# Kernel optimization log

Hardware: AMD Instinct MI355X
Metric: run time of the kernel (lower is better)

Reference implementation:

```python
import jax, jax.numpy as jnp
import numpy as np
import math

EMBED = 256
HEADS = 4
HEAD_DIM = EMBED // HEADS
OUT_DIM = 256
LN_EPS = 1e-5


def _qkv_init(key):
    # diagonal-domination init from Galerkin Transformer (Cao): U(-spread,spread)*gain + delta*I
    spread = math.sqrt(3.0 / EMBED)
    gain, delta = 0.01, 0.01
    w = jax.random.uniform(key, (EMBED, EMBED), minval=-spread, maxval=spread) * gain
    return w + delta * jnp.eye(EMBED, dtype=w.dtype)


def setup_inputs() -> dict:
    key = jax.random.key(0)
    ks = jax.random.split(key, 6)
    seq = jax.random.normal(ks[0], (4, 8192, EMBED), dtype=jnp.float32)
    wq = _qkv_init(ks[1])
    wk = _qkv_init(ks[2])
    wv = _qkv_init(ks[3])
    # nn.Linear default init for wo
    bound = 1.0 / math.sqrt(EMBED)
    wo = jax.random.uniform(ks[4], (OUT_DIM, EMBED), minval=-bound, maxval=bound)
    bo = jax.random.uniform(ks[5], (OUT_DIM,), minval=-bound, maxval=bound)
    ln_k_g = jnp.ones((HEAD_DIM,), jnp.float32)
    ln_k_b = jnp.zeros((HEAD_DIM,), jnp.float32)
    ln_v_g = jnp.ones((HEAD_DIM,), jnp.float32)
    ln_v_b = jnp.zeros((HEAD_DIM,), jnp.float32)
    return {"seq": seq, "wq": wq, "wk": wk, "wv": wv, "wo": wo, "bo": bo,
            "ln_k_g": ln_k_g, "ln_k_b": ln_k_b, "ln_v_g": ln_v_g, "ln_v_b": ln_v_b}


def _layer_norm(x, g, b):
    mu = jnp.mean(x, axis=-1, keepdims=True)
    var = jnp.mean(jnp.square(x - mu), axis=-1, keepdims=True)
    return (x - mu) * jax.lax.rsqrt(var + LN_EPS) * g + b


def _split_heads(x, B, S):
    # [B, S, E] -> [B, H, S, D]
    return x.reshape(B, S, HEADS, HEAD_DIM).transpose(0, 2, 1, 3)


def reference(seq, wq, wk, wv, wo, bo, ln_k_g, ln_k_b, ln_v_g, ln_v_b):
    B, S, _ = seq.shape
    q = _split_heads(seq @ wq.T, B, S)
    k = _split_heads(seq @ wk.T, B, S)
    v = _split_heads(seq @ wv.T, B, S)
    k = _layer_norm(k, ln_k_g, ln_k_b)
    v = _layer_norm(v, ln_v_g, ln_v_b)
    # Galerkin (softmax-free) attention: Q @ (K^T V) / n  -- O(n d^2)
    kv = jnp.einsum('bhsd,bhse->bhde', k, v) / S   # [B,H,D,D]
    ga = jnp.einsum('bhsd,bhde->bhse', q, kv)       # [B,H,S,D]
    ga = ga.transpose(0, 2, 1, 3).reshape(B, S, EMBED)
    return ga @ wo.T + bo
```

## Files before the change

### kernel.cpp

```cpp
#include <hip/hip_runtime.h>
#include <stdint.h>


#define EMBED 256
#define SEQ   8192
#define LN_EPS 1e-5f

using bf16x8 = __attribute__((ext_vector_type(8))) short;
using bf16x4 = __attribute__((ext_vector_type(4))) short;
using f32x4  = __attribute__((ext_vector_type(4))) float;

static __device__ __forceinline__ short f2bf(float f) {
  uint32_t x = __float_as_uint(f);
  uint32_t r = x + 0x7fffu + ((x >> 16) & 1u);
  return (short)(r >> 16);
}
static __device__ __forceinline__ float bf2f(uint32_t u) {
  return __uint_as_float(u << 16);
}

#define MFMA16(a, b, c) __builtin_amdgcn_mfma_f32_16x16x32_bf16((a), (b), (c), 0, 0, 0)

template <int ROWS>
static __device__ __forceinline__ void stage_x(char* smem, const float* __restrict__ src, int tid) {
#pragma unroll
  for (int i = 0; i < ROWS / 8; ++i) {
    int g = tid + i * 256;
    int row = g >> 5, c16 = g & 31;
    const f32x4* p = (const f32x4*)(src + row * EMBED + c16 * 8);
    f32x4 f0 = p[0], f1 = p[1];
    bf16x8 v;
    v[0] = f2bf(f0[0]); v[1] = f2bf(f0[1]); v[2] = f2bf(f0[2]); v[3] = f2bf(f0[3]);
    v[4] = f2bf(f1[0]); v[5] = f2bf(f1[1]); v[6] = f2bf(f1[2]); v[7] = f2bf(f1[3]);
    *(bf16x8*)(smem + row * 512 + ((c16 * 16) ^ ((row & 7) << 4))) = v;
  }
}

__global__ void gka_prep(const float* __restrict__ wq, const float* __restrict__ wk,
                         const float* __restrict__ wv, const float* __restrict__ wo,
                         unsigned short* __restrict__ wkf, unsigned short* __restrict__ wvf,
                         unsigned short* __restrict__ wqt, unsigned short* __restrict__ wob) {
  int blk = blockIdx.x, tid = threadIdx.x;
  if (blk < 64) {
    int g = (blk & 31) * 256 + tid;
    const float* W = (blk < 32) ? wk : wv;
    unsigned short* D = (blk < 32) ? wkf : wvf;
    int wid = g >> 11, kk = (g >> 8) & 7, n = (g >> 6) & 3, ln = g & 63;
    int row = wid * 64 + n * 16 + (ln & 15);
    int c0 = kk * 32 + (ln >> 4) * 8;
    const f32x4* p = (const f32x4*)(W + row * 256 + c0);
    f32x4 f0 = p[0], f1 = p[1];
    bf16x8 v;
    v[0] = f2bf(f0[0]); v[1] = f2bf(f0[1]); v[2] = f2bf(f0[2]); v[3] = f2bf(f0[3]);
    v[4] = f2bf(f1[0]); v[5] = f2bf(f1[1]); v[6] = f2bf(f1[2]); v[7] = f2bf(f1[3]);
    *(bf16x8*)(D + g * 8) = v;
  } else if (blk < 320) {
    int e = (blk - 64) * 256 + tid;
    int i = e >> 8, j = e & 255;
    wqt[e] = (unsigned short)f2bf(wq[j * 256 + i]);
  } else {
    int e = (blk - 320) * 256 + tid;
    wob[e] = (unsigned short)f2bf(wo[e]);
  }
}

__global__ __launch_bounds__(256, 2)
void gka_kv(const float* __restrict__ seq,
            const unsigned short* __restrict__ wkf, const unsigned short* __restrict__ wvf,
            const float* __restrict__ lkg, const float* __restrict__ lkb,
            const float* __restrict__ lvg, const float* __restrict__ lvb,
            unsigned short* __restrict__ P) {
  __shared__ char smem[65536];
  const int tid = threadIdx.x;
  const int lane = tid & 63;
  const int wid = tid >> 6;
  const int l15 = lane & 15, l4 = lane >> 4, l7 = lane & 7;
  const int tile = blockIdx.x;
  const int b = tile >> 7;
  const int ptile = tile & 127;

  stage_x<64>(smem, seq + (size_t)(b * SEQ + ptile * 64) * EMBED, tid);
  __syncthreads();

#pragma unroll
  for (int mat = 0; mat < 2; ++mat) {
    const unsigned short* Wf = mat ? wvf : wkf;
    const float* gp = mat ? lvg : lkg;
    const float* bp = mat ? lvb : lkb;
    float gv[4], bv[4];
#pragma unroll
    for (int n = 0; n < 4; ++n) { gv[n] = gp[n * 16 + l15]; bv[n] = bp[n * 16 + l15]; }

    f32x4 acc[4][4];
#pragma unroll
    for (int m = 0; m < 4; ++m)
#pragma unroll
      for (int n = 0; n < 4; ++n) acc[m][n] = (f32x4)0.0f;

#pragma unroll
    for (int kk = 0; kk < 8; ++kk) {
      bf16x8 af[4], bw[4];
#pragma unroll
      for (int m = 0; m < 4; ++m) {
        int row = m * 16 + l15;
        af[m] = *(const bf16x8*)(smem + row * 512 + ((kk * 64 + l4 * 16) ^ (l7 << 4)));
      }
#pragma unroll
      for (int n = 0; n < 4; ++n)
        bw[n] = *(const bf16x8*)(Wf + ((((wid * 8 + kk) * 4 + n) * 64 + lane) << 3));
#pragma unroll
      for (int m = 0; m < 4; ++m)
#pragma unroll
        for (int n = 0; n < 4; ++n)
          acc[m][n] = MFMA16(af[m], bw[n], acc[m][n]);
    }

    if (mat == 1) __syncthreads();

    char* T = smem + (mat ? 0 : 32768) + wid * 8192;
#pragma unroll
    for (int m = 0; m < 4; ++m) {
      float mu[4], rs[4];
#pragma unroll
      for (int r = 0; r < 4; ++r) {
        float s1 = 0.f, s2 = 0.f;
#pragma unroll
        for (int n = 0; n < 4; ++n) { float x = acc[m][n][r]; s1 += x; s2 += x * x; }
#pragma unroll
        for (int msk = 1; msk < 16; msk <<= 1) {
          s1 += __shfl_xor(s1, msk);
          s2 += __shfl_xor(s2, msk);
        }
        mu[r] = s1 * (1.f / 64.f);
        float var = s2 * (1.f / 64.f) - mu[r] * mu[r];
        rs[r] = rsqrtf(var + LN_EPS);
      }
#pragma unroll
      for (int n = 0; n < 4; ++n) {
        bf16x4 pk;
#pragma unroll
        for (int r = 0; r < 4; ++r)
          pk[r] = f2bf((acc[m][n][r] - mu[r]) * rs[r] * gv[n] + bv[n]);
        int d = n * 16 + l15;
        int sb = m * 32 + l4 * 8;
        *(bf16x4*)(T + d * 128 + (sb ^ (l7 << 4))) = pk;
      }
    }
  }

  __syncthreads();

  f32x4 a2[4][4];
#pragma unroll
  for (int fd = 0; fd < 4; ++fd)
#pragma unroll
    for (int n = 0; n < 4; ++n) a2[fd][n] = (f32x4)0.0f;

#pragma unroll
  for (int kk = 0; kk < 2; ++kk) {
    bf16x8 ak[4], bv2[4];
#pragma unroll
    for (int fd = 0; fd < 4; ++fd) {
      int d = fd * 16 + l15;
      ak[fd] = *(const bf16x8*)(smem + 32768 + wid * 8192 + d * 128 +
                                ((kk * 64 + l4 * 16) ^ (l7 << 4)));
    }
#pragma unroll
    for (int n = 0; n < 4; ++n) {
      int e = n * 16 + l15;
      bv2[n] = *(const bf16x8*)(smem + wid * 8192 + e * 128 +
                                ((kk * 64 + l4 * 16) ^ (l7 << 4)));
    }
#pragma unroll
    for (int fd = 0; fd < 4; ++fd)
#pragma unroll
      for (int n = 0; n < 4; ++n)
        a2[fd][n] = MFMA16(ak[fd], bv2[n], a2[fd][n]);
  }

  unsigned short* Ph = P + ((size_t)((b * 128 + ptile) * 4 + wid) << 12);
#pragma unroll
  for (int fd = 0; fd < 4; ++fd)
#pragma unroll
    for (int n = 0; n < 4; ++n) {
      bf16x4 pk;
#pragma unroll
      for (int r = 0; r < 4; ++r) pk[r] = f2bf(a2[fd][n][r]);
      *(bf16x4*)(Ph + (fd * 4 + n) * 256 + lane * 4) = pk;
    }
}

__global__ __launch_bounds__(128)
void gka_red(const unsigned short* __restrict__ P, float* __restrict__ kvf) {
  int q = blockIdx.x * 128 + threadIdx.x;
  int b = q >> 12, h = (q >> 10) & 3, t4 = q & 1023;
  const unsigned short* p0 = P + ((size_t)(b * 128) * 4 + h) * 4096 + t4 * 4;
  float s0 = 0.f, s1 = 0.f, s2 = 0.f, s3 = 0.f;
#pragma unroll 4
  for (int p = 0; p < 128; ++p) {
    uint2 u = *(const uint2*)(p0 + (size_t)p * 16384);
    s0 += bf2f(u.x & 0xffffu); s1 += bf2f(u.x >> 16);
    s2 += bf2f(u.y & 0xffffu); s3 += bf2f(u.y >> 16);
  }
  f32x4 r; r[0] = s0; r[1] = s1; r[2] = s2; r[3] = s3;
  *(f32x4*)(kvf + ((b * 4 + h) << 12) + t4 * 4) = r;
}

__global__ __launch_bounds__(256, 2)
void gka_m1(const float* __restrict__ kvf, const unsigned short* __restrict__ wob,
            unsigned short* __restrict__ m1t) {
  const int tid = threadIdx.x;
  const int lane = tid & 63;
  const int wid = tid >> 6;
  const int l15 = lane & 15, l4 = lane >> 4;
  const int blk = blockIdx.x;
  const int b = blk >> 2, h = blk & 3;
  const float invS = 1.f / (float)SEQ;
  const float* kvh = kvf + ((b * 4 + h) << 12);

  f32x4 acc[4][4];
#pragma unroll
  for (int m = 0; m < 4; ++m)
#pragma unroll
    for (int n = 0; n < 4; ++n) acc[m][n] = (f32x4)0.0f;

#pragma unroll
  for (int kk = 0; kk < 2; ++kk) {
    bf16x8 af[4], bw[4];
#pragma unroll
    for (int m = 0; m < 4; ++m) {
      int base = (m * 4 + kk * 2 + (l4 >> 1)) * 256 +
                 ((l15 >> 2) * 16 + (l4 & 1) * 8) * 4 + (l15 & 3);
      bf16x8 v;
#pragma unroll
      for (int j = 0; j < 8; ++j) v[j] = f2bf(kvh[base + j * 4] * invS);
      af[m] = v;
    }
#pragma unroll
    for (int n = 0; n < 4; ++n) {
      int o = wid * 64 + n * 16 + l15;
      bw[n] = *(const bf16x8*)(wob + o * 256 + h * 64 + kk * 32 + l4 * 8);
    }
#pragma unroll
    for (int m = 0; m < 4; ++m)
#pragma unroll
      for (int n = 0; n < 4; ++n)
        acc[m][n] = MFMA16(af[m], bw[n], acc[m][n]);
  }
#pragma unroll
  for (int m = 0; m < 4; ++m)
#pragma unroll
    for (int n = 0; n < 4; ++n) {
      int o = wid * 64 + n * 16 + l15;
      int j0 = h * 64 + m * 16 + l4 * 4;
      bf16x4 pk;
#pragma unroll
      for (int r = 0; r < 4; ++r) pk[r] = f2bf(acc[m][n][r]);
      *(bf16x4*)(m1t + (size_t)(b * 256 + o) * 256 + j0) = pk;
    }
}

__global__ __launch_bounds__(512, 2)
void gka_wc(const unsigned short* __restrict__ wqt, const unsigned short* __restrict__ m1t,
            unsigned short* __restrict__ wcf) {
  const int tid = threadIdx.x;
  const int lane = tid & 63;
  const int wid = tid >> 6;
  const int wm = wid >> 2, wn = wid & 3;
  const int l15 = lane & 15, l4 = lane >> 4;
  const int blk = blockIdx.x;
  const int b = blk >> 1, ih = blk & 1;

  f32x4 acc[4][4];
#pragma unroll
  for (int m = 0; m < 4; ++m)
#pragma unroll
    for (int n = 0; n < 4; ++n) acc[m][n] = (f32x4)0.0f;

#pragma unroll
  for (int kk = 0; kk < 8; ++kk) {
    bf16x8 af[4], bw[4];
#pragma unroll
    for (int m = 0; m < 4; ++m) {
      int i = ih * 128 + wm * 64 + m * 16 + l15;
      af[m] = *(const bf16x8*)(wqt + i * 256 + kk * 32 + l4 * 8);
    }
#pragma unroll
    for (int n = 0; n < 4; ++n) {
      int o = wn * 64 + n * 16 + l15;
      bw[n] = *(const bf16x8*)(m1t + (size_t)(b * 256 + o) * 256 + kk * 32 + l4 * 8);
    }
#pragma unroll
    for (int m = 0; m < 4; ++m)
#pragma unroll
      for (int n = 0; n < 4; ++n)
        acc[m][n] = MFMA16(af[m], bw[n], acc[m][n]);
  }
#pragma unroll
  for (int m = 0; m < 4; ++m)
#pragma unroll
    for (int n = 0; n < 4; ++n) {
      int kko = ih * 4 + wm * 2 + (m >> 1);
      int laneo = ((m & 1) * 2 + (l4 >> 1)) * 16 + l15;
      int jo = (l4 & 1) * 4;
      bf16x4 pk;
#pragma unroll
      for (int r = 0; r < 4; ++r) pk[r] = f2bf(acc[m][n][r]);
      *(bf16x4*)(wcf + ((size_t)b << 16) +
                 (((((wn * 8 + kko) * 4 + n) * 64) + laneo) << 3) + jo) = pk;
    }
}

__global__ __launch_bounds__(256, 4)
void gka_out(const float* __restrict__ seq, const unsigned short* __restrict__ wcf,
             const float* __restrict__ bo, float* __restrict__ out) {
  __shared__ char smem[16384];
  const int tid = threadIdx.x;
  const int lane = tid & 63;
  const int wid = tid >> 6;
  const int l15 = lane & 15, l4 = lane >> 4, l7 = lane & 7;
  const int tile = blockIdx.x;
  const int b = tile >> 8;
  const int srow = (tile & 255) * 32;

  stage_x<32>(smem, seq + (size_t)(b * SEQ + srow) * EMBED, tid);

  const unsigned short* Wf = wcf + ((size_t)b << 16);
  float bov[4];
#pragma unroll
  for (int n = 0; n < 4; ++n) bov[n] = bo[wid * 64 + n * 16 + l15];

  f32x4 acc[2][4];
#pragma unroll
  for (int m = 0; m < 2; ++m)
#pragma unroll
    for (int n = 0; n < 4; ++n) acc[m][n] = (f32x4)0.0f;

  __syncthreads();

#pragma unroll
  for (int kk = 0; kk < 8; ++kk) {
    bf16x8 af[2], bw[4];
#pragma unroll
    for (int m = 0; m < 2; ++m) {
      int row = m * 16 + l15;
      af[m] = *(const bf16x8*)(smem + row * 512 + ((kk * 64 + l4 * 16) ^ (l7 << 4)));
    }
#pragma unroll
    for (int n = 0; n < 4; ++n)
      bw[n] = *(const bf16x8*)(Wf + ((((wid * 8 + kk) * 4 + n) * 64 + lane) << 3));
#pragma unroll
    for (int m = 0; m < 2; ++m)
#pragma unroll
      for (int n = 0; n < 4; ++n)
        acc[m][n] = MFMA16(af[m], bw[n], acc[m][n]);
  }

  float* dst = out + (size_t)(b * SEQ + srow) * EMBED;
#pragma unroll
  for (int m = 0; m < 2; ++m)
#pragma unroll
    for (int n = 0; n < 4; ++n)
#pragma unroll
      for (int r = 0; r < 4; ++r)
        dst[(size_t)(m * 16 + l4 * 4 + r) * EMBED + wid * 64 + n * 16 + l15] =
            acc[m][n][r] + bov[n];
}

extern "C" void kernel_launch(void* const* d_in, const int* in_sizes, int n_in,
                              void* d_out, int out_size, void* d_ws, size_t ws_size,
                              hipStream_t stream) {
  const float* seq = (const float*)d_in[0];
  const float* wq  = (const float*)d_in[1];
  const float* wk  = (const float*)d_in[2];
  const float* wv  = (const float*)d_in[3];
  const float* wo  = (const float*)d_in[4];
  const float* bo  = (const float*)d_in[5];
  const float* lkg = (const float*)d_in[6];
  const float* lkb = (const float*)d_in[7];
  const float* lvg = (const float*)d_in[8];
  const float* lvb = (const float*)d_in[9];
  float* out = (float*)d_out;
  char* ws = (char*)d_ws;

  unsigned short* wkf = (unsigned short*)(ws + 0);
  unsigned short* wvf = (unsigned short*)(ws + 131072);
  unsigned short* wqt = (unsigned short*)(ws + 262144);
  unsigned short* wob = (unsigned short*)(ws + 393216);
  float*          kvf = (float*)(ws + 524288);
  unsigned short* m1t = (unsigned short*)(ws + 786432);
  unsigned short* wcf = (unsigned short*)(ws + 1310720);
  unsigned short* P   = (unsigned short*)d_out;

  gka_prep<<<576, 256, 0, stream>>>(wq, wk, wv, wo, wkf, wvf, wqt, wob);
  gka_kv<<<512, 256, 0, stream>>>(seq, wkf, wvf, lkg, lkb, lvg, lvb, P);
  gka_red<<<128, 128, 0, stream>>>(P, kvf);
  gka_m1<<<16, 256, 0, stream>>>(kvf, wob, m1t);
  gka_wc<<<8, 512, 0, stream>>>(wqt, m1t, wcf);
  gka_out<<<1024, 256, 0, stream>>>(seq, wcf, bo, out);
}
```

Baseline: 79.78 us.

## Tile wq transpose, split partial reduction, fuse wo conversion, drop LDS staging in output

```diff
diff --git a/kernel.cpp b/kernel.cpp
--- a/kernel.cpp
+++ b/kernel.cpp
@@ -1,4 +1,5 @@
 #include <hip/hip_runtime.h>
+#include <hip/hip_bf16.h>
 #include <stdint.h>
 
 
@@ -11,9 +12,8 @@
 using f32x4  = __attribute__((ext_vector_type(4))) float;
 
 static __device__ __forceinline__ short f2bf(float f) {
-  uint32_t x = __float_as_uint(f);
-  uint32_t r = x + 0x7fffu + ((x >> 16) & 1u);
-  return (short)(r >> 16);
+  __hip_bfloat16 h = __float2bfloat16(f);
+  return __builtin_bit_cast(short, h);
 }
 static __device__ __forceinline__ float bf2f(uint32_t u) {
   return __uint_as_float(u << 16);
@@ -21,10 +21,9 @@
 
 #define MFMA16(a, b, c) __builtin_amdgcn_mfma_f32_16x16x32_bf16((a), (b), (c), 0, 0, 0)
 
-template <int ROWS>
 static __device__ __forceinline__ void stage_x(char* smem, const float* __restrict__ src, int tid) {
 #pragma unroll
-  for (int i = 0; i < ROWS / 8; ++i) {
+  for (int i = 0; i < 8; ++i) {
     int g = tid + i * 256;
     int row = g >> 5, c16 = g & 31;
     const f32x4* p = (const f32x4*)(src + row * EMBED + c16 * 8);
@@ -37,9 +36,10 @@
 }
 
 __global__ void gka_prep(const float* __restrict__ wq, const float* __restrict__ wk,
-                         const float* __restrict__ wv, const float* __restrict__ wo,
+                         const float* __restrict__ wv,
                          unsigned short* __restrict__ wkf, unsigned short* __restrict__ wvf,
-                         unsigned short* __restrict__ wqt, unsigned short* __restrict__ wob) {
+                         unsigned short* __restrict__ wqt) {
+  __shared__ unsigned short T[64 * 66];
   int blk = blockIdx.x, tid = threadIdx.x;
   if (blk < 64) {
     int g = (blk & 31) * 256 + tid;
@@ -54,13 +54,26 @@
     v[0] = f2bf(f0[0]); v[1] = f2bf(f0[1]); v[2] = f2bf(f0[2]); v[3] = f2bf(f0[3]);
     v[4] = f2bf(f1[0]); v[5] = f2bf(f1[1]); v[6] = f2bf(f1[2]); v[7] = f2bf(f1[3]);
     *(bf16x8*)(D + g * 8) = v;
-  } else if (blk < 320) {
-    int e = (blk - 64) * 256 + tid;
-    int i = e >> 8, j = e & 255;
-    wqt[e] = (unsigned short)f2bf(wq[j * 256 + i]);
-  } else {
-    int e = (blk - 320) * 256 + tid;
-    wob[e] = (unsigned short)f2bf(wo[e]);
+    return;
+  }
+  int t = blk - 64, ti = t >> 2, tj = t & 3;
+#pragma unroll
+  for (int it = 0; it < 4; ++it) {
+    int g = tid + it * 256;
+    int jl = g >> 4, g4 = g & 15;
+    f32x4 f = *(const f32x4*)(wq + (tj * 64 + jl) * 256 + ti * 64 + g4 * 4);
+#pragma unroll
+    for (int q = 0; q < 4; ++q) T[jl * 66 + g4 * 4 + q] = (unsigned short)f2bf(f[q]);
+  }
+  __syncthreads();
+#pragma unroll
+  for (int it = 0; it < 2; ++it) {
+    int g = tid + it * 256;
+    int il = g >> 3, j8 = g & 7;
+    bf16x8 v;
+#pragma unroll
+    for (int q = 0; q < 8; ++q) v[q] = (short)T[(j8 * 8 + q) * 66 + il];
+    *(bf16x8*)(wqt + (ti * 64 + il) * 256 + tj * 64 + j8 * 8) = v;
   }
 }
 
@@ -79,7 +92,7 @@
   const int b = tile >> 7;
   const int ptile = tile & 127;
 
-  stage_x<64>(smem, seq + (size_t)(b * SEQ + ptile * 64) * EMBED, tid);
+  stage_x(smem, seq + (size_t)(b * SEQ + ptile * 64) * EMBED, tid);
   __syncthreads();
 
 #pragma unroll
@@ -190,24 +203,34 @@
     }
 }
 
-__global__ __launch_bounds__(128)
+__global__ __launch_bounds__(256)
 void gka_red(const unsigned short* __restrict__ P, float* __restrict__ kvf) {
-  int q = blockIdx.x * 128 + threadIdx.x;
-  int b = q >> 12, h = (q >> 10) & 3, t4 = q & 1023;
-  const unsigned short* p0 = P + ((size_t)(b * 128) * 4 + h) * 4096 + t4 * 4;
+  int gtid = blockIdx.x * 256 + threadIdx.x;
+  int chunk = gtid & 7;
+  int qid = gtid >> 3;
+  int b = qid >> 12, h = (qid >> 10) & 3, t4 = qid & 1023;
+  const unsigned short* p0 = P + ((size_t)(b * 512 + h) << 12) + t4 * 4;
   float s0 = 0.f, s1 = 0.f, s2 = 0.f, s3 = 0.f;
-#pragma unroll 4
-  for (int p = 0; p < 128; ++p) {
-    uint2 u = *(const uint2*)(p0 + (size_t)p * 16384);
+#pragma unroll
+  for (int s = 0; s < 16; ++s) {
+    int p = chunk * 16 + s;
+    uint2 u = *(const uint2*)(p0 + ((size_t)p << 14));
     s0 += bf2f(u.x & 0xffffu); s1 += bf2f(u.x >> 16);
     s2 += bf2f(u.y & 0xffffu); s3 += bf2f(u.y >> 16);
   }
-  f32x4 r; r[0] = s0; r[1] = s1; r[2] = s2; r[3] = s3;
-  *(f32x4*)(kvf + ((b * 4 + h) << 12) + t4 * 4) = r;
+#pragma unroll
+  for (int msk = 1; msk < 8; msk <<= 1) {
+    s0 += __shfl_xor(s0, msk); s1 += __shfl_xor(s1, msk);
+    s2 += __shfl_xor(s2, msk); s3 += __shfl_xor(s3, msk);
+  }
+  if (chunk == 0) {
+    f32x4 r; r[0] = s0; r[1] = s1; r[2] = s2; r[3] = s3;
+    *(f32x4*)(kvf + (qid << 2)) = r;
+  }
 }
 
 __global__ __launch_bounds__(256, 2)
-void gka_m1(const float* __restrict__ kvf, const unsigned short* __restrict__ wob,
+void gka_m1(const float* __restrict__ kvf, const float* __restrict__ wo,
             unsigned short* __restrict__ m1t) {
   const int tid = threadIdx.x;
   const int lane = tid & 63;
@@ -239,7 +262,12 @@
 #pragma unroll
     for (int n = 0; n < 4; ++n) {
       int o = wid * 64 + n * 16 + l15;
-      bw[n] = *(const bf16x8*)(wob + o * 256 + h * 64 + kk * 32 + l4 * 8);
+      const f32x4* wp = (const f32x4*)(wo + (size_t)o * 256 + h * 64 + kk * 32 + l4 * 8);
+      f32x4 w0 = wp[0], w1 = wp[1];
+      bf16x8 v;
+      v[0] = f2bf(w0[0]); v[1] = f2bf(w0[1]); v[2] = f2bf(w0[2]); v[3] = f2bf(w0[3]);
+      v[4] = f2bf(w1[0]); v[5] = f2bf(w1[1]); v[6] = f2bf(w1[2]); v[7] = f2bf(w1[3]);
+      bw[n] = v;
     }
 #pragma unroll
     for (int m = 0; m < 4; ++m)
@@ -314,17 +342,15 @@
 __global__ __launch_bounds__(256, 4)
 void gka_out(const float* __restrict__ seq, const unsigned short* __restrict__ wcf,
              const float* __restrict__ bo, float* __restrict__ out) {
-  __shared__ char smem[16384];
   const int tid = threadIdx.x;
   const int lane = tid & 63;
   const int wid = tid >> 6;
-  const int l15 = lane & 15, l4 = lane >> 4, l7 = lane & 7;
+  const int l15 = lane & 15, l4 = lane >> 4;
   const int tile = blockIdx.x;
   const int b = tile >> 8;
   const int srow = (tile & 255) * 32;
 
-  stage_x<32>(smem, seq + (size_t)(b * SEQ + srow) * EMBED, tid);
-
+  const float* X = seq + (size_t)(b * SEQ + srow) * EMBED;
   const unsigned short* Wf = wcf + ((size_t)b << 16);
   float bov[4];
 #pragma unroll
@@ -336,15 +362,17 @@
 #pragma unroll
     for (int n = 0; n < 4; ++n) acc[m][n] = (f32x4)0.0f;
 
-  __syncthreads();
-
 #pragma unroll
   for (int kk = 0; kk < 8; ++kk) {
     bf16x8 af[2], bw[4];
 #pragma unroll
     for (int m = 0; m < 2; ++m) {
-      int row = m * 16 + l15;
-      af[m] = *(const bf16x8*)(smem + row * 512 + ((kk * 64 + l4 * 16) ^ (l7 << 4)));
+      const f32x4* p = (const f32x4*)(X + (m * 16 + l15) * EMBED + kk * 32 + l4 * 8);
+      f32x4 f0 = p[0], f1 = p[1];
+      bf16x8 v;
+      v[0] = f2bf(f0[0]); v[1] = f2bf(f0[1]); v[2] = f2bf(f0[2]); v[3] = f2bf(f0[3]);
+      v[4] = f2bf(f1[0]); v[5] = f2bf(f1[1]); v[6] = f2bf(f1[2]); v[7] = f2bf(f1[3]);
+      af[m] = v;
     }
 #pragma unroll
     for (int n = 0; n < 4; ++n)
@@ -386,16 +414,15 @@
   unsigned short* wkf = (unsigned short*)(ws + 0);
   unsigned short* wvf = (unsigned short*)(ws + 131072);
   unsigned short* wqt = (unsigned short*)(ws + 262144);
-  unsigned short* wob = (unsigned short*)(ws + 393216);
   float*          kvf = (float*)(ws + 524288);
   unsigned short* m1t = (unsigned short*)(ws + 786432);
   unsigned short* wcf = (unsigned short*)(ws + 1310720);
   unsigned short* P   = (unsigned short*)d_out;
 
-  gka_prep<<<576, 256, 0, stream>>>(wq, wk, wv, wo, wkf, wvf, wqt, wob);
+  gka_prep<<<80, 256, 0, stream>>>(wq, wk, wv, wkf, wvf, wqt);
   gka_kv<<<512, 256, 0, stream>>>(seq, wkf, wvf, lkg, lkb, lvg, lvb, P);
-  gka_red<<<128, 128, 0, stream>>>(P, kvf);
-  gka_m1<<<16, 256, 0, stream>>>(kvf, wob, m1t);
+  gka_red<<<512, 256, 0, stream>>>(P, kvf);
+  gka_m1<<<16, 256, 0, stream>>>(kvf, wo, m1t);
   gka_wc<<<8, 512, 0, stream>>>(wqt, m1t, wcf);
   gka_out<<<1024, 256, 0, stream>>>(seq, wcf, bo, out);
 }
```

Result: slower. 82.90 us (+3.9%).
